# Kernel tuning notes

Measured on AMD Instinct MI355X. Metric: run time of the kernel, lower is better.

Reference implementation:

```python
import jax, jax.numpy as jnp
import numpy as np


def _gcn_norm(edge_index, num_nodes, dtype):
    # PyG GCNConv.norm: add self-loops (weight 1), symmetric deg^{-1/2} normalization
    row, col = edge_index[0], edge_index[1]
    loop = jnp.arange(num_nodes, dtype=row.dtype)
    row = jnp.concatenate([row, loop])
    col = jnp.concatenate([col, loop])
    ew = jnp.ones(row.shape[0], dtype=dtype)
    deg = jax.ops.segment_sum(ew, row, num_segments=num_nodes)
    dis = jnp.where(deg > 0, jax.lax.rsqrt(deg), 0.0)
    norm = dis[row] * ew * dis[col]
    return row, col, norm


def _masked_gcn_conv(x, row, col, norm, sigma, W, b, num_nodes):
    # mask_features: edge gather -> diff/sigma -> square -> scatter-add -> exp mask
    h = (x[col] - x[row]) / sigma            # [E, F]
    h = norm[:, None] * h * h                # [E, F]
    mask = jax.ops.segment_sum(h, row, num_segments=num_nodes)        # [N, F]
    deg = jax.ops.segment_sum(jnp.ones_like(norm), row, num_segments=num_nodes)  # degree(source), >=1 due to self-loops
    x = x * jnp.exp(-mask / deg[:, None])
    # GCNConv: linear transform then normalized aggregation source->target
    xw = x @ W                               # [N, O]
    out = jax.ops.segment_sum(norm[:, None] * xw[row], col, num_segments=num_nodes)
    return out + b


def setup_inputs() -> dict:
    key = jax.random.key(0)
    ks = jax.random.split(key, 8)
    N, E, F, H, C = 100000, 1600000, 128, 64, 40
    g = 1.414  # xavier gain used for sigma
    return {
        "x": jax.random.normal(ks[0], (N, F), jnp.float32),
        "edge_index": jax.random.randint(ks[1], (2, E), 0, N, jnp.int64),
        "sigma1": jax.random.uniform(ks[2], (1, F), jnp.float32, -1.0, 1.0) * (g * np.sqrt(6.0 / (1 + F))),
        "W1": jax.random.normal(ks[3], (F, H), jnp.float32) * (1.0 / np.sqrt(F)),
        "b1": jnp.zeros((H,), jnp.float32),
        "sigma2": jax.random.uniform(ks[4], (1, H), jnp.float32, -1.0, 1.0) * (g * np.sqrt(6.0 / (1 + H))),
        "W2": jax.random.normal(ks[5], (H, C), jnp.float32) * (1.0 / np.sqrt(H)),
        "b2": jnp.zeros((C,), jnp.float32),
    }


def reference(x, edge_index, sigma1, W1, b1, sigma2, W2, b2):
    N = x.shape[0]
    row, col, norm = _gcn_norm(edge_index, N, x.dtype)
    x = _masked_gcn_conv(x, row, col, norm, sigma1, W1, b1, N)
    x = jax.nn.relu(x)
    # dropout is identity in eval mode
    x = _masked_gcn_conv(x, row, col, norm, sigma2, W2, b2, N)
    return jax.nn.log_softmax(x, axis=1)
```

## Files before the change

### kernel.cpp

```cpp
#include <hip/hip_runtime.h>
#include <cmath>

constexpr int F1 = 128;
constexpr int H  = 64;
constexpr int NC = 40;
constexpr int NXCD = 8;

constexpr int SCAN_TPB = 256;
constexpr int SCAN_IPT = 8;
constexpr int SCAN_EPB = SCAN_TPB * SCAN_IPT;

__device__ inline unsigned short f2bf(float f) {
    union { float f; unsigned u; } v; v.f = f;
    unsigned r = (v.u + 0x7FFFu + ((v.u >> 16) & 1u)) >> 16;
    return (unsigned short)r;
}
__device__ inline float bflo(unsigned p) {
    union { float f; unsigned u; } v; v.u = p << 16; return v.f;
}
__device__ inline float bfhi(unsigned p) {
    union { float f; unsigned u; } v; v.u = p & 0xFFFF0000u; return v.f;
}

__global__ void isg_kernel(const float* __restrict__ s1, float* __restrict__ i1,
                           const float* __restrict__ s2, float* __restrict__ i2) {
    int i = threadIdx.x;
    if (i < F1) i1[i] = 1.0f / s1[i];
    if (i < H)  i2[i] = 1.0f / s2[i];
}

__global__ void prep_u_kernel(const float* __restrict__ x, const float* __restrict__ isg,
                              unsigned short* __restrict__ u, size_t n8, int F) {
    size_t idx = (size_t)blockIdx.x * blockDim.x + threadIdx.x;
    if (idx >= n8) return;
    size_t base = idx * 8;
    int fk = (int)(base % (size_t)F);
    float4 a0 = *(const float4*)&x[base];
    float4 a1 = *(const float4*)&x[base + 4];
    float4 s0 = *(const float4*)&isg[fk];
    float4 s1 = *(const float4*)&isg[fk + 4];
    uint4 p;
    p.x = (unsigned)f2bf(a0.x * s0.x) | ((unsigned)f2bf(a0.y * s0.y) << 16);
    p.y = (unsigned)f2bf(a0.z * s0.z) | ((unsigned)f2bf(a0.w * s0.w) << 16);
    p.z = (unsigned)f2bf(a1.x * s1.x) | ((unsigned)f2bf(a1.y * s1.y) << 16);
    p.w = (unsigned)f2bf(a1.z * s1.z) | ((unsigned)f2bf(a1.w * s1.w) << 16);
    *(uint4*)&u[base] = p;
}

__global__ void count8_kernel(const int* __restrict__ row, const int* __restrict__ col,
                              int* __restrict__ cntO, int* __restrict__ cntI,
                              int E, int chunk, int stride) {
    int p = blockIdx.x & (NXCD - 1);
    int gid = blockIdx.x >> 3;
    unsigned lo = (unsigned)(p * chunk);
    for (int e = gid * blockDim.x + threadIdx.x; e < E; e += stride) {
        int r = row[e], c = col[e];
        if ((unsigned)r - lo < (unsigned)chunk) atomicAdd(&cntO[r], 1);
        if ((unsigned)c - lo < (unsigned)chunk) atomicAdd(&cntI[c], 1);
    }
}

__global__ void scan_partial_kernel(const int* __restrict__ cnt, int* __restrict__ bsum, int M) {
    __shared__ int red[SCAN_TPB];
    int t = threadIdx.x;
    int i0 = blockIdx.x * SCAN_EPB + t * SCAN_IPT;
    int s = 0;
#pragma unroll
    for (int k = 0; k < SCAN_IPT; ++k) {
        int i = i0 + k;
        if (i < M) s += cnt[i];
    }
    red[t] = s;
    __syncthreads();
    for (int off = SCAN_TPB / 2; off > 0; off >>= 1) {
        if (t < off) red[t] += red[t + off];
        __syncthreads();
    }
    if (t == 0) bsum[blockIdx.x] = red[0];
}

__global__ void scan_offsets_kernel(int* __restrict__ bsum, int nb,
                                    int* __restrict__ rowptrO, int* __restrict__ rowptrI,
                                    int N, int E) {
    __shared__ int sh[1024];
    int t = threadIdx.x;
    sh[t] = (t < nb) ? bsum[t] : 0;
    __syncthreads();
    for (int off = 1; off < 1024; off <<= 1) {
        int v = (t >= off) ? sh[t - off] : 0;
        __syncthreads();
        sh[t] += v;
        __syncthreads();
    }
    if (t < nb) bsum[t] = (t > 0) ? sh[t - 1] : 0;
    if (t == 0) { rowptrO[N] = E; rowptrI[N] = E; }
}

__global__ void scan_final_kernel(int* __restrict__ cntO, int* __restrict__ cntI,
                                  const int* __restrict__ bsum,
                                  int* __restrict__ rowptrO, int* __restrict__ rowptrI,
                                  float* __restrict__ dis, int N, int E) {
    __shared__ int sh[SCAN_TPB];
    int t = threadIdx.x;
    int M = 2 * N;
    const int* cnt = cntO;
    int i0 = blockIdx.x * SCAN_EPB + t * SCAN_IPT;
    int cv[SCAN_IPT], pre[SCAN_IPT];
    int run = 0;
#pragma unroll
    for (int k = 0; k < SCAN_IPT; ++k) {
        int i = i0 + k;
        cv[k] = (i < M) ? cnt[i] : 0;
        pre[k] = run;
        run += cv[k];
    }
    sh[t] = run;
    __syncthreads();
    for (int off = 1; off < SCAN_TPB; off <<= 1) {
        int v = (t >= off) ? sh[t - off] : 0;
        __syncthreads();
        sh[t] += v;
        __syncthreads();
    }
    int toff = ((t > 0) ? sh[t - 1] : 0) + bsum[blockIdx.x];
#pragma unroll
    for (int k = 0; k < SCAN_IPT; ++k) {
        int i = i0 + k;
        if (i < M) {
            int val = toff + pre[k];
            if (i < N) {
                rowptrO[i] = val;
                cntO[i] = val;
                dis[i] = rsqrtf((float)(cv[k] + 1));
            } else {
                rowptrI[i - N] = val - E;
                cntI[i - N] = val - E;
            }
        }
    }
}

__global__ void build8_kernel(const int* __restrict__ row, const int* __restrict__ col,
                              int* __restrict__ curO, int* __restrict__ curI,
                              int* __restrict__ adjO, int* __restrict__ adjI,
                              int E, int chunk, int stride) {
    int p = blockIdx.x & (NXCD - 1);
    int gid = blockIdx.x >> 3;
    unsigned lo = (unsigned)(p * chunk);
    for (int e = gid * blockDim.x + threadIdx.x; e < E; e += stride) {
        int r = row[e], c = col[e];
        if ((unsigned)r - lo < (unsigned)chunk) adjO[atomicAdd(&curO[r], 1)] = c;
        if ((unsigned)c - lo < (unsigned)chunk) adjI[atomicAdd(&curI[c], 1)] = r;
    }
}

template<int F, int O, int R>
__global__ void fused_mask_gemm_kernel(const int* __restrict__ rowptr, const int* __restrict__ adj,
                                       const float* __restrict__ dis, const float* __restrict__ x,
                                       const unsigned short* __restrict__ u,
                                       const float* __restrict__ W,
                                       float* __restrict__ Y, int N) {
    constexpr int NT = R * 64;
    constexpr int G = F / 8;
    constexpr int NPI = 64 / G;
    __shared__ __align__(16) float Ws[F * O];
    __shared__ __align__(16) float Xs[R][F];
    int tid = threadIdx.x;
    for (int i = tid; i < F * O; i += NT) Ws[i] = W[i];

    int w = tid >> 6, lane = tid & 63;
    int h = lane / G;
    int j = lane % G;
    int r = blockIdx.x * R + w;
    if (r < N) {
        int beg = rowptr[r], end = rowptr[r + 1];
        float dr = dis[r];
        float inv_deg = 1.0f / (float)(end - beg + 1);
        float xr[8], ur[8], acc[8];
        {
            float4 a0 = *(const float4*)&x[(size_t)r * F + 8 * j];
            float4 a1 = *(const float4*)&x[(size_t)r * F + 8 * j + 4];
            xr[0] = a0.x; xr[1] = a0.y; xr[2] = a0.z; xr[3] = a0.w;
            xr[4] = a1.x; xr[5] = a1.y; xr[6] = a1.z; xr[7] = a1.w;
            uint4 rr = *(const uint4*)&u[(size_t)r * F + 8 * j];
            ur[0] = bflo(rr.x); ur[1] = bfhi(rr.x);
            ur[2] = bflo(rr.y); ur[3] = bfhi(rr.y);
            ur[4] = bflo(rr.z); ur[5] = bfhi(rr.z);
            ur[6] = bflo(rr.w); ur[7] = bfhi(rr.w);
        }
#pragma unroll
        for (int k = 0; k < 8; ++k) acc[k] = 0.0f;
        for (int base = beg; base < end; base += 64) {
            int nn = min(64, end - base);
            int cl = 0; float dl = 0.0f;
            if (base + lane < end) { cl = adj[base + lane]; dl = dis[cl]; }
            for (int t = 0; t < nn; t += NPI) {
                int i = t + h;
                bool valid = i < nn;
                int ii = valid ? i : 0;
                int c = __shfl(cl, ii);
                float nrm = valid ? dr * __shfl(dl, ii) : 0.0f;
                uint4 raw = *(const uint4*)&u[(size_t)c * F + 8 * j];
                float uc[8];
                uc[0] = bflo(raw.x); uc[1] = bfhi(raw.x);
                uc[2] = bflo(raw.y); uc[3] = bfhi(raw.y);
                uc[4] = bflo(raw.z); uc[5] = bfhi(raw.z);
                uc[6] = bflo(raw.w); uc[7] = bfhi(raw.w);
#pragma unroll
                for (int k = 0; k < 8; ++k) {
                    float d = uc[k] - ur[k];
                    acc[k] = fmaf(nrm * d, d, acc[k]);
                }
            }
        }
#pragma unroll
        for (int off = G; off < 64; off <<= 1) {
#pragma unroll
            for (int k = 0; k < 8; ++k) acc[k] += __shfl_xor(acc[k], off);
        }
        if (h == 0) {
            float xm[8];
#pragma unroll
            for (int k = 0; k < 8; ++k) xm[k] = xr[k] * expf(-acc[k] * inv_deg);
            *(float4*)&Xs[w][8 * j]     = make_float4(xm[0], xm[1], xm[2], xm[3]);
            *(float4*)&Xs[w][8 * j + 4] = make_float4(xm[4], xm[5], xm[6], xm[7]);
        }
    } else {
        if (h == 0) {
            *(float4*)&Xs[w][8 * j]     = make_float4(0.f, 0.f, 0.f, 0.f);
            *(float4*)&Xs[w][8 * j + 4] = make_float4(0.f, 0.f, 0.f, 0.f);
        }
    }
    __syncthreads();

    int row0 = blockIdx.x * R;
    for (int idx = tid; idx < R * O; idx += NT) {
        int rr = idx / O, o = idx % O;
        if (row0 + rr < N) {
            float acc = 0.0f;
#pragma unroll
            for (int f = 0; f < F; ++f) acc = fmaf(Xs[rr][f], Ws[f * O + o], acc);
            Y[(size_t)(row0 + rr) * O + o] = acc;
        }
    }
}

template<int O, int MODE>
__global__ void agg_gather_kernel(const int* __restrict__ rowptr, const int* __restrict__ adj,
                                  const float* __restrict__ dis, const float* __restrict__ xw,
                                  const float* __restrict__ bias, float* __restrict__ out,
                                  unsigned short* __restrict__ u2, const float* __restrict__ isg2,
                                  int N) {
    int c = blockIdx.x * (blockDim.x >> 6) + (threadIdx.x >> 6);
    if (c >= N) return;
    int lane = threadIdx.x & 63;
    int j = lane & 15, h = lane >> 4;
    bool active = (4 * j < O);
    int beg = rowptr[c], end = rowptr[c + 1];
    float dc = dis[c];
    float4 a = {0.f, 0.f, 0.f, 0.f};
    if (h == 0 && active) {
        float4 v = *(const float4*)&xw[(size_t)c * O + 4 * j];
        a.x = dc * dc * v.x; a.y = dc * dc * v.y;
        a.z = dc * dc * v.z; a.w = dc * dc * v.w;
    }
    for (int base = beg; base < end; base += 64) {
        int nn = min(64, end - base);
        int rl = 0; float dl = 0.0f;
        if (base + lane < end) { rl = adj[base + lane]; dl = dis[rl]; }
        for (int t = 0; t < nn; t += 4) {
            int i = t + h;
            bool valid = i < nn;
            int ii = valid ? i : 0;
            int rr = __shfl(rl, ii);
            float nrm = valid ? dc * __shfl(dl, ii) : 0.0f;
            if (active) {
                float4 v = *(const float4*)&xw[(size_t)rr * O + 4 * j];
                a.x = fmaf(nrm, v.x, a.x);
                a.y = fmaf(nrm, v.y, a.y);
                a.z = fmaf(nrm, v.z, a.z);
                a.w = fmaf(nrm, v.w, a.w);
            }
        }
    }
    a.x += __shfl_xor(a.x, 16); a.x += __shfl_xor(a.x, 32);
    a.y += __shfl_xor(a.y, 16); a.y += __shfl_xor(a.y, 32);
    a.z += __shfl_xor(a.z, 16); a.z += __shfl_xor(a.z, 32);
    a.w += __shfl_xor(a.w, 16); a.w += __shfl_xor(a.w, 32);
    if (MODE == 0) {
        if (h == 0 && active) {
            float4 bb = *(const float4*)&bias[4 * j];
            float4 o4;
            o4.x = fmaxf(a.x + bb.x, 0.0f);
            o4.y = fmaxf(a.y + bb.y, 0.0f);
            o4.z = fmaxf(a.z + bb.z, 0.0f);
            o4.w = fmaxf(a.w + bb.w, 0.0f);
            *(float4*)&out[(size_t)c * O + 4 * j] = o4;
            float4 s4 = *(const float4*)&isg2[4 * j];
            uint2 p;
            p.x = (unsigned)f2bf(o4.x * s4.x) | ((unsigned)f2bf(o4.y * s4.y) << 16);
            p.y = (unsigned)f2bf(o4.z * s4.z) | ((unsigned)f2bf(o4.w * s4.w) << 16);
            *(uint2*)&u2[(size_t)c * O + 4 * j] = p;
        }
    } else {
        float4 v = {-INFINITY, -INFINITY, -INFINITY, -INFINITY};
        if (active) {
            float4 bb = *(const float4*)&bias[4 * j];
            v.x = a.x + bb.x; v.y = a.y + bb.y; v.z = a.z + bb.z; v.w = a.w + bb.w;
        }
        float m = fmaxf(fmaxf(v.x, v.y), fmaxf(v.z, v.w));
#pragma unroll
        for (int off = 8; off > 0; off >>= 1) m = fmaxf(m, __shfl_xor(m, off));
        float s = active ? (expf(v.x - m) + expf(v.y - m) + expf(v.z - m) + expf(v.w - m)) : 0.0f;
#pragma unroll
        for (int off = 8; off > 0; off >>= 1) s += __shfl_xor(s, off);
        float mls = m + logf(s);
        if (h == 0 && active) {
            float4 o4 = {v.x - mls, v.y - mls, v.z - mls, v.w - mls};
            *(float4*)&out[(size_t)c * O + 4 * j] = o4;
        }
    }
}

extern "C" void kernel_launch(void* const* d_in, const int* in_sizes, int n_in,
                              void* d_out, int out_size, void* d_ws, size_t ws_size,
                              hipStream_t stream) {
    const float* x    = (const float*)d_in[0];
    const int*   ei   = (const int*)  d_in[1];
    const float* sig1 = (const float*)d_in[2];
    const float* W1   = (const float*)d_in[3];
    const float* b1   = (const float*)d_in[4];
    const float* sig2 = (const float*)d_in[5];
    const float* W2   = (const float*)d_in[6];
    const float* b2   = (const float*)d_in[7];
    float* out = (float*)d_out;

    const int N = in_sizes[0] / F1;
    const int E = in_sizes[1] / 2;
    const int* row = ei;
    const int* col = ei + E;

    char* w = (char*)d_ws;
    auto alloc = [&](size_t bytes) { void* q = w; w += (bytes + 255) & ~255ull; return q; };
    int*   cntO    = (int*)  alloc((size_t)2 * N * 4);
    int*   cntI    = cntO + N;
    int*   rowptrO = (int*)  alloc((size_t)(N + 1) * 4);
    int*   rowptrI = (int*)  alloc((size_t)(N + 1) * 4);
    int*   adjO    = (int*)  alloc((size_t)E * 4);
    int*   adjI    = (int*)  alloc((size_t)E * 4);
    float* dis     = (float*)alloc((size_t)N * 4);
    float* isg1    = (float*)alloc(F1 * 4);
    float* isg2    = (float*)alloc(H * 4);
    int*   bsum    = (int*)  alloc(1024 * 4);
    unsigned short* u1 = (unsigned short*)alloc((size_t)N * F1 * 2);
    unsigned short* u2 = (unsigned short*)alloc((size_t)N * H * 2);
    float* bufXW   = (float*)alloc((size_t)N * H * 4);
    float* bufH    = (float*)alloc((size_t)N * H * 4);
    float* bufXW2  = (float*)u1;

    const int B = 256;
    const int chunk = (N + NXCD - 1) / NXCD;
    const int WPP = 1024;
    const int stride8 = WPP * B;
    dim3 g8(NXCD * WPP);
    const int M = 2 * N;
    const int nb = (M + SCAN_EPB - 1) / SCAN_EPB;

    hipMemsetAsync(cntO, 0, (size_t)2 * N * 4, stream);
    isg_kernel<<<1, 128, 0, stream>>>(sig1, isg1, sig2, isg2);
    prep_u_kernel<<<(int)(((size_t)N * F1 / 8 + B - 1) / B), B, 0, stream>>>(x, isg1, u1, (size_t)N * F1 / 8, F1);
    count8_kernel<<<g8, B, 0, stream>>>(row, col, cntO, cntI, E, chunk, stride8);
    scan_partial_kernel<<<nb, SCAN_TPB, 0, stream>>>(cntO, bsum, M);
    scan_offsets_kernel<<<1, 1024, 0, stream>>>(bsum, nb, rowptrO, rowptrI, N, E);
    scan_final_kernel<<<nb, SCAN_TPB, 0, stream>>>(cntO, cntI, bsum, rowptrO, rowptrI, dis, N, E);
    build8_kernel<<<g8, B, 0, stream>>>(row, col, cntO, cntI, adjO, adjI, E, chunk, stride8);

    fused_mask_gemm_kernel<F1, H, 8><<<(N + 7) / 8, 512, 0, stream>>>(rowptrO, adjO, dis, x, u1, W1, bufXW, N);
    agg_gather_kernel<H, 0><<<(N + 3) / 4, B, 0, stream>>>(rowptrI, adjI, dis, bufXW, b1, bufH, u2, isg2, N);

    fused_mask_gemm_kernel<H, NC, 8><<<(N + 7) / 8, 512, 0, stream>>>(rowptrO, adjO, dis, bufH, u2, W2, bufXW2, N);
    agg_gather_kernel<NC, 1><<<(N + 3) / 4, B, 0, stream>>>(rowptrI, adjI, dis, bufXW2, b2, out, nullptr, nullptr, N);
}
```

Before: 672.5 us.

## Store XW in bf16, transpose W in LDS, and specialize aggregation kernels

The GEMM output XW is now written as packed bf16 instead of fp32, which halves the bytes gathered per edge in the aggregation kernels. The mini-GEMM stage loads W transposed and padded into shared memory and has each lane compute one output column with float4 LDS reads. The aggregation and mask loops drop the 64-wide adjacency prefetch with shuffles and index adj and dis directly per edge. The generic aggregation kernel is split into separate layer-1 (ReLU plus u2 packing) and layer-2 (log-softmax) kernels with wider per-lane loads, at the cost of extra bf16 rounding error in XW.

```diff
diff --git a/kernel.cpp b/kernel.cpp
--- a/kernel.cpp
+++ b/kernel.cpp
@@ -12,14 +12,13 @@
 
 __device__ inline unsigned short f2bf(float f) {
     union { float f; unsigned u; } v; v.f = f;
-    unsigned r = (v.u + 0x7FFFu + ((v.u >> 16) & 1u)) >> 16;
-    return (unsigned short)r;
-}
-__device__ inline float bflo(unsigned p) {
-    union { float f; unsigned u; } v; v.u = p << 16; return v.f;
-}
-__device__ inline float bfhi(unsigned p) {
-    union { float f; unsigned u; } v; v.u = p & 0xFFFF0000u; return v.f;
+    return (unsigned short)((v.u + 0x7FFFu + ((v.u >> 16) & 1u)) >> 16);
+}
+__device__ inline float bflo(unsigned p) { union { float f; unsigned u; } v; v.u = p << 16; return v.f; }
+__device__ inline float bfhi(unsigned p) { union { float f; unsigned u; } v; v.u = p & 0xFFFF0000u; return v.f; }
+__device__ inline void unpack8(uint4 raw, float* d) {
+    d[0] = bflo(raw.x); d[1] = bfhi(raw.x); d[2] = bflo(raw.y); d[3] = bfhi(raw.y);
+    d[4] = bflo(raw.z); d[5] = bfhi(raw.z); d[6] = bflo(raw.w); d[7] = bfhi(raw.w);
 }
 
 __global__ void isg_kernel(const float* __restrict__ s1, float* __restrict__ i1,
@@ -159,167 +158,174 @@
                                        const float* __restrict__ dis, const float* __restrict__ x,
                                        const unsigned short* __restrict__ u,
                                        const float* __restrict__ W,
-                                       float* __restrict__ Y, int N) {
+                                       unsigned short* __restrict__ Ybf, int N) {
     constexpr int NT = R * 64;
     constexpr int G = F / 8;
     constexpr int NPI = 64 / G;
-    __shared__ __align__(16) float Ws[F * O];
-    __shared__ __align__(16) float Xs[R][F];
+    constexpr int FP = F + 4;
+    __shared__ __align__(16) float WsT[O * FP];
+    __shared__ __align__(16) float Xs[R][FP];
     int tid = threadIdx.x;
-    for (int i = tid; i < F * O; i += NT) Ws[i] = W[i];
-
+    for (int i = tid; i < F * O; i += NT) {
+        int f = i / O, o = i - f * O;
+        WsT[o * FP + f] = W[i];
+    }
     int w = tid >> 6, lane = tid & 63;
-    int h = lane / G;
-    int j = lane % G;
+    int h = lane / G, j = lane % G;
     int r = blockIdx.x * R + w;
     if (r < N) {
         int beg = rowptr[r], end = rowptr[r + 1];
         float dr = dis[r];
         float inv_deg = 1.0f / (float)(end - beg + 1);
-        float xr[8], ur[8], acc[8];
-        {
+        float ur[8], acc[8];
+        unpack8(*(const uint4*)&u[(size_t)r * F + 8 * j], ur);
+#pragma unroll
+        for (int k = 0; k < 8; ++k) acc[k] = 0.0f;
+        for (int t = beg; t < end; t += NPI) {
+            int e = t + h;
+            bool valid = e < end;
+            int c = adj[valid ? e : beg];
+            float nrm = valid ? dr * dis[c] : 0.0f;
+            float uc[8];
+            unpack8(*(const uint4*)&u[(size_t)c * F + 8 * j], uc);
+#pragma unroll
+            for (int k = 0; k < 8; ++k) {
+                float d = uc[k] - ur[k];
+                acc[k] = fmaf(nrm * d, d, acc[k]);
+            }
+        }
+#pragma unroll
+        for (int off = G; off < 64; off <<= 1) {
+#pragma unroll
+            for (int k = 0; k < 8; ++k) acc[k] += __shfl_xor(acc[k], off);
+        }
+        if (h == 0) {
             float4 a0 = *(const float4*)&x[(size_t)r * F + 8 * j];
             float4 a1 = *(const float4*)&x[(size_t)r * F + 8 * j + 4];
-            xr[0] = a0.x; xr[1] = a0.y; xr[2] = a0.z; xr[3] = a0.w;
-            xr[4] = a1.x; xr[5] = a1.y; xr[6] = a1.z; xr[7] = a1.w;
-            uint4 rr = *(const uint4*)&u[(size_t)r * F + 8 * j];
-            ur[0] = bflo(rr.x); ur[1] = bfhi(rr.x);
-            ur[2] = bflo(rr.y); ur[3] = bfhi(rr.y);
-            ur[4] = bflo(rr.z); ur[5] = bfhi(rr.z);
-            ur[6] = bflo(rr.w); ur[7] = bfhi(rr.w);
-        }
-#pragma unroll
-        for (int k = 0; k < 8; ++k) acc[k] = 0.0f;
-        for (int base = beg; base < end; base += 64) {
-            int nn = min(64, end - base);
-            int cl = 0; float dl = 0.0f;
-            if (base + lane < end) { cl = adj[base + lane]; dl = dis[cl]; }
-            for (int t = 0; t < nn; t += NPI) {
-                int i = t + h;
-                bool valid = i < nn;
-                int ii = valid ? i : 0;
-                int c = __shfl(cl, ii);
-                float nrm = valid ? dr * __shfl(dl, ii) : 0.0f;
-                uint4 raw = *(const uint4*)&u[(size_t)c * F + 8 * j];
-                float uc[8];
-                uc[0] = bflo(raw.x); uc[1] = bfhi(raw.x);
-                uc[2] = bflo(raw.y); uc[3] = bfhi(raw.y);
-                uc[4] = bflo(raw.z); uc[5] = bfhi(raw.z);
-                uc[6] = bflo(raw.w); uc[7] = bfhi(raw.w);
-#pragma unroll
-                for (int k = 0; k < 8; ++k) {
-                    float d = uc[k] - ur[k];
-                    acc[k] = fmaf(nrm * d, d, acc[k]);
-                }
-            }
-        }
-#pragma unroll
-        for (int off = G; off < 64; off <<= 1) {
-#pragma unroll
-            for (int k = 0; k < 8; ++k) acc[k] += __shfl_xor(acc[k], off);
-        }
-        if (h == 0) {
-            float xm[8];
-#pragma unroll
-            for (int k = 0; k < 8; ++k) xm[k] = xr[k] * expf(-acc[k] * inv_deg);
+            float xm[8] = {a0.x, a0.y, a0.z, a0.w, a1.x, a1.y, a1.z, a1.w};
+#pragma unroll
+            for (int k = 0; k < 8; ++k) xm[k] *= expf(-acc[k] * inv_deg);
             *(float4*)&Xs[w][8 * j]     = make_float4(xm[0], xm[1], xm[2], xm[3]);
             *(float4*)&Xs[w][8 * j + 4] = make_float4(xm[4], xm[5], xm[6], xm[7]);
         }
-    } else {
-        if (h == 0) {
-            *(float4*)&Xs[w][8 * j]     = make_float4(0.f, 0.f, 0.f, 0.f);
-            *(float4*)&Xs[w][8 * j + 4] = make_float4(0.f, 0.f, 0.f, 0.f);
-        }
     }
     __syncthreads();
-
-    int row0 = blockIdx.x * R;
-    for (int idx = tid; idx < R * O; idx += NT) {
-        int rr = idx / O, o = idx % O;
-        if (row0 + rr < N) {
-            float acc = 0.0f;
-#pragma unroll
-            for (int f = 0; f < F; ++f) acc = fmaf(Xs[rr][f], Ws[f * O + o], acc);
-            Y[(size_t)(row0 + rr) * O + o] = acc;
-        }
-    }
-}
-
-template<int O, int MODE>
-__global__ void agg_gather_kernel(const int* __restrict__ rowptr, const int* __restrict__ adj,
-                                  const float* __restrict__ dis, const float* __restrict__ xw,
-                                  const float* __restrict__ bias, float* __restrict__ out,
-                                  unsigned short* __restrict__ u2, const float* __restrict__ isg2,
-                                  int N) {
+    if (r < N && lane < O) {
+        float acc = 0.0f;
+#pragma unroll
+        for (int fq = 0; fq < F / 4; ++fq) {
+            float4 xs = *(const float4*)&Xs[w][4 * fq];
+            float4 ws = *(const float4*)&WsT[lane * FP + 4 * fq];
+            acc = fmaf(xs.x, ws.x, acc); acc = fmaf(xs.y, ws.y, acc);
+            acc = fmaf(xs.z, ws.z, acc); acc = fmaf(xs.w, ws.w, acc);
+        }
+        float other = __shfl_xor(acc, 1);
+        if (!(lane & 1)) {
+            unsigned p = (unsigned)f2bf(acc) | ((unsigned)f2bf(other) << 16);
+            *(unsigned*)&Ybf[(size_t)r * O + lane] = p;
+        }
+    }
+}
+
+__global__ void agg_relu_kernel(const int* __restrict__ rowptr, const int* __restrict__ adj,
+                                const float* __restrict__ dis, const unsigned short* __restrict__ ybf,
+                                const float* __restrict__ bias, float* __restrict__ h1,
+                                unsigned short* __restrict__ u2, const float* __restrict__ isg2, int N) {
     int c = blockIdx.x * (blockDim.x >> 6) + (threadIdx.x >> 6);
     if (c >= N) return;
     int lane = threadIdx.x & 63;
-    int j = lane & 15, h = lane >> 4;
-    bool active = (4 * j < O);
+    int h = lane >> 3, j = lane & 7;
     int beg = rowptr[c], end = rowptr[c + 1];
     float dc = dis[c];
-    float4 a = {0.f, 0.f, 0.f, 0.f};
-    if (h == 0 && active) {
-        float4 v = *(const float4*)&xw[(size_t)c * O + 4 * j];
-        a.x = dc * dc * v.x; a.y = dc * dc * v.y;
-        a.z = dc * dc * v.z; a.w = dc * dc * v.w;
-    }
-    for (int base = beg; base < end; base += 64) {
-        int nn = min(64, end - base);
-        int rl = 0; float dl = 0.0f;
-        if (base + lane < end) { rl = adj[base + lane]; dl = dis[rl]; }
-        for (int t = 0; t < nn; t += 4) {
-            int i = t + h;
-            bool valid = i < nn;
-            int ii = valid ? i : 0;
-            int rr = __shfl(rl, ii);
-            float nrm = valid ? dc * __shfl(dl, ii) : 0.0f;
-            if (active) {
-                float4 v = *(const float4*)&xw[(size_t)rr * O + 4 * j];
-                a.x = fmaf(nrm, v.x, a.x);
-                a.y = fmaf(nrm, v.y, a.y);
-                a.z = fmaf(nrm, v.z, a.z);
-                a.w = fmaf(nrm, v.w, a.w);
-            }
-        }
-    }
-    a.x += __shfl_xor(a.x, 16); a.x += __shfl_xor(a.x, 32);
-    a.y += __shfl_xor(a.y, 16); a.y += __shfl_xor(a.y, 32);
-    a.z += __shfl_xor(a.z, 16); a.z += __shfl_xor(a.z, 32);
-    a.w += __shfl_xor(a.w, 16); a.w += __shfl_xor(a.w, 32);
-    if (MODE == 0) {
-        if (h == 0 && active) {
-            float4 bb = *(const float4*)&bias[4 * j];
-            float4 o4;
-            o4.x = fmaxf(a.x + bb.x, 0.0f);
-            o4.y = fmaxf(a.y + bb.y, 0.0f);
-            o4.z = fmaxf(a.z + bb.z, 0.0f);
-            o4.w = fmaxf(a.w + bb.w, 0.0f);
-            *(float4*)&out[(size_t)c * O + 4 * j] = o4;
-            float4 s4 = *(const float4*)&isg2[4 * j];
-            uint2 p;
-            p.x = (unsigned)f2bf(o4.x * s4.x) | ((unsigned)f2bf(o4.y * s4.y) << 16);
-            p.y = (unsigned)f2bf(o4.z * s4.z) | ((unsigned)f2bf(o4.w * s4.w) << 16);
-            *(uint2*)&u2[(size_t)c * O + 4 * j] = p;
-        }
-    } else {
-        float4 v = {-INFINITY, -INFINITY, -INFINITY, -INFINITY};
-        if (active) {
-            float4 bb = *(const float4*)&bias[4 * j];
-            v.x = a.x + bb.x; v.y = a.y + bb.y; v.z = a.z + bb.z; v.w = a.w + bb.w;
-        }
-        float m = fmaxf(fmaxf(v.x, v.y), fmaxf(v.z, v.w));
-#pragma unroll
-        for (int off = 8; off > 0; off >>= 1) m = fmaxf(m, __shfl_xor(m, off));
-        float s = active ? (expf(v.x - m) + expf(v.y - m) + expf(v.z - m) + expf(v.w - m)) : 0.0f;
-#pragma unroll
-        for (int off = 8; off > 0; off >>= 1) s += __shfl_xor(s, off);
-        float mls = m + logf(s);
-        if (h == 0 && active) {
-            float4 o4 = {v.x - mls, v.y - mls, v.z - mls, v.w - mls};
-            *(float4*)&out[(size_t)c * O + 4 * j] = o4;
-        }
-    }
+    float acc[8];
+#pragma unroll
+    for (int k = 0; k < 8; ++k) acc[k] = 0.0f;
+    for (int t = beg; t < end; t += 8) {
+        int e = t + h;
+        bool valid = e < end;
+        int rr = adj[valid ? e : beg];
+        float nrm = valid ? dc * dis[rr] : 0.0f;
+        float v[8];
+        unpack8(*(const uint4*)&ybf[(size_t)rr * H + 8 * j], v);
+#pragma unroll
+        for (int k = 0; k < 8; ++k) acc[k] = fmaf(nrm, v[k], acc[k]);
+    }
+#pragma unroll
+    for (int off = 8; off < 64; off <<= 1) {
+#pragma unroll
+        for (int k = 0; k < 8; ++k) acc[k] += __shfl_xor(acc[k], off);
+    }
+    if (h == 0) {
+        float sv[8];
+        unpack8(*(const uint4*)&ybf[(size_t)c * H + 8 * j], sv);
+        float4 b0 = *(const float4*)&bias[8 * j];
+        float4 b1v = *(const float4*)&bias[8 * j + 4];
+        float bb[8] = {b0.x, b0.y, b0.z, b0.w, b1v.x, b1v.y, b1v.z, b1v.w};
+        float4 s0 = *(const float4*)&isg2[8 * j];
+        float4 s1 = *(const float4*)&isg2[8 * j + 4];
+        float sg[8] = {s0.x, s0.y, s0.z, s0.w, s1.x, s1.y, s1.z, s1.w};
+        float hv[8];
+        float d2 = dc * dc;
+#pragma unroll
+        for (int k = 0; k < 8; ++k) hv[k] = fmaxf(fmaf(d2, sv[k], acc[k]) + bb[k], 0.0f);
+        *(float4*)&h1[(size_t)c * H + 8 * j]     = make_float4(hv[0], hv[1], hv[2], hv[3]);
+        *(float4*)&h1[(size_t)c * H + 8 * j + 4] = make_float4(hv[4], hv[5], hv[6], hv[7]);
+        uint4 p;
+        p.x = (unsigned)f2bf(hv[0] * sg[0]) | ((unsigned)f2bf(hv[1] * sg[1]) << 16);
+        p.y = (unsigned)f2bf(hv[2] * sg[2]) | ((unsigned)f2bf(hv[3] * sg[3]) << 16);
+        p.z = (unsigned)f2bf(hv[4] * sg[4]) | ((unsigned)f2bf(hv[5] * sg[5]) << 16);
+        p.w = (unsigned)f2bf(hv[6] * sg[6]) | ((unsigned)f2bf(hv[7] * sg[7]) << 16);
+        *(uint4*)&u2[(size_t)c * H + 8 * j] = p;
+    }
+}
+
+__global__ void agg_lsm_kernel(const int* __restrict__ rowptr, const int* __restrict__ adj,
+                               const float* __restrict__ dis, const unsigned short* __restrict__ ybf,
+                               const float* __restrict__ bias, float* __restrict__ out, int N) {
+    int c = blockIdx.x * (blockDim.x >> 6) + (threadIdx.x >> 6);
+    if (c >= N) return;
+    int lane = threadIdx.x & 63;
+    int h = lane >> 4, j = lane & 15;
+    bool active = j < 10;
+    int beg = rowptr[c], end = rowptr[c + 1];
+    float dc = dis[c];
+    float a[4] = {0.f, 0.f, 0.f, 0.f};
+    for (int t = beg; t < end; t += 4) {
+        int e = t + h;
+        bool valid = e < end;
+        int rr = adj[valid ? e : beg];
+        float nrm = (valid && active) ? dc * dis[rr] : 0.0f;
+        uint2 raw = active ? *(const uint2*)&ybf[(size_t)rr * NC + 4 * j] : make_uint2(0u, 0u);
+        a[0] = fmaf(nrm, bflo(raw.x), a[0]);
+        a[1] = fmaf(nrm, bfhi(raw.x), a[1]);
+        a[2] = fmaf(nrm, bflo(raw.y), a[2]);
+        a[3] = fmaf(nrm, bfhi(raw.y), a[3]);
+    }
+#pragma unroll
+    for (int off = 16; off < 64; off <<= 1) {
+#pragma unroll
+        for (int k = 0; k < 4; ++k) a[k] += __shfl_xor(a[k], off);
+    }
+    bool wr = (h == 0) && active;
+    float v[4] = {-INFINITY, -INFINITY, -INFINITY, -INFINITY};
+    if (wr) {
+        uint2 sr = *(const uint2*)&ybf[(size_t)c * NC + 4 * j];
+        float sv[4] = {bflo(sr.x), bfhi(sr.x), bflo(sr.y), bfhi(sr.y)};
+        float4 bb = *(const float4*)&bias[4 * j];
+        float b4[4] = {bb.x, bb.y, bb.z, bb.w};
+        float d2 = dc * dc;
+#pragma unroll
+        for (int k = 0; k < 4; ++k) v[k] = fmaf(d2, sv[k], a[k]) + b4[k];
+    }
+    float m = fmaxf(fmaxf(v[0], v[1]), fmaxf(v[2], v[3]));
+#pragma unroll
+    for (int off = 8; off > 0; off >>= 1) m = fmaxf(m, __shfl_xor(m, off));
+    float s = wr ? (expf(v[0] - m) + expf(v[1] - m) + expf(v[2] - m) + expf(v[3] - m)) : 0.0f;
+#pragma unroll
+    for (int off = 8; off > 0; off >>= 1) s += __shfl_xor(s, off);
+    float mls = m + logf(s);
+    if (wr)
+        *(float4*)&out[(size_t)c * NC + 4 * j] = make_float4(v[0] - mls, v[1] - mls, v[2] - mls, v[3] - mls);
 }
 
 extern "C" void kernel_launch(void* const* d_in, const int* in_sizes, int n_in,
@@ -352,11 +358,11 @@
     float* isg1    = (float*)alloc(F1 * 4);
     float* isg2    = (float*)alloc(H * 4);
     int*   bsum    = (int*)  alloc(1024 * 4);
-    unsigned short* u1 = (unsigned short*)alloc((size_t)N * F1 * 2);
-    unsigned short* u2 = (unsigned short*)alloc((size_t)N * H * 2);
-    float* bufXW   = (float*)alloc((size_t)N * H * 4);
-    float* bufH    = (float*)alloc((size_t)N * H * 4);
-    float* bufXW2  = (float*)u1;
+    unsigned short* u1   = (unsigned short*)alloc((size_t)N * F1 * 2);
+    unsigned short* u2   = (unsigned short*)alloc((size_t)N * H * 2);
+    unsigned short* ybf1 = (unsigned short*)alloc((size_t)N * H * 2);
+    float* h1      = (float*)alloc((size_t)N * H * 4);
+    unsigned short* ybf2 = u1;
 
     const int B = 256;
     const int chunk = (N + NXCD - 1) / NXCD;
@@ -375,9 +381,9 @@
     scan_final_kernel<<<nb, SCAN_TPB, 0, stream>>>(cntO, cntI, bsum, rowptrO, rowptrI, dis, N, E);
     build8_kernel<<<g8, B, 0, stream>>>(row, col, cntO, cntI, adjO, adjI, E, chunk, stride8);
 
-    fused_mask_gemm_kernel<F1, H, 8><<<(N + 7) / 8, 512, 0, stream>>>(rowptrO, adjO, dis, x, u1, W1, bufXW, N);
-    agg_gather_kernel<H, 0><<<(N + 3) / 4, B, 0, stream>>>(rowptrI, adjI, dis, bufXW, b1, bufH, u2, isg2, N);
-
-    fused_mask_gemm_kernel<H, NC, 8><<<(N + 7) / 8, 512, 0, stream>>>(rowptrO, adjO, dis, bufH, u2, W2, bufXW2, N);
-    agg_gather_kernel<NC, 1><<<(N + 3) / 4, B, 0, stream>>>(rowptrI, adjI, dis, bufXW2, b2, out, nullptr, nullptr, N);
-}
+    fused_mask_gemm_kernel<F1, H, 8><<<(N + 7) / 8, 512, 0, stream>>>(rowptrO, adjO, dis, x, u1, W1, ybf1, N);
+    agg_relu_kernel<<<(N + 3) / 4, B, 0, stream>>>(rowptrI, adjI, dis, ybf1, b1, h1, u2, isg2, N);
+
+    fused_mask_gemm_kernel<H, NC, 8><<<(N + 7) / 8, 512, 0, stream>>>(rowptrO, adjO, dis, h1, u2, W2, ybf2, N);
+    agg_lsm_kernel<<<(N + 3) / 4, B, 0, stream>>>(rowptrI, adjI, dis, ybf2, b2, out, N);
+}
```

Result: slower. 689.7 us (+2.6%).
